# Kernel tuning notes

Measured on AMD Instinct MI355X. Metric: run time of the kernel, lower is better.

Reference implementation:

```python
import jax, jax.numpy as jnp
import numpy as np

B, L, H, C = 1, 512, 1024, 2


def setup_inputs() -> dict:
    key = jax.random.key(0)
    k1, k2, k3 = jax.random.split(key, 3)
    lm_output = jax.random.normal(k1, (B, L, H), dtype=jnp.float32)
    # torch Linear weight layout: [out_features, in_features]
    W1 = jax.random.normal(k2, (H, 2 * H), dtype=jnp.float32) * 0.02
    b1 = jnp.zeros((H,), dtype=jnp.float32)
    W2 = jax.random.normal(k3, (C, H), dtype=jnp.float32) * 0.02
    b2 = jnp.zeros((C,), dtype=jnp.float32)
    return {"lm_output": lm_output, "W1": W1, "b1": b1, "W2": W2, "b2": b2}


def reference(lm_output, W1, b1, W2, b2):
    # pair_emb[b,i,j] = concat(lm_output[b,j], lm_output[b,i])
    # Linear(concat(a,b)) decomposes: split W1 into the halves acting on each part.
    Wa = W1[:, :H]  # acts on lm_output_a (the j / column token)
    Wb = W1[:, H:]  # acts on lm_output_b (the i / row token)
    a_proj = jnp.einsum('blh,oh->blo', lm_output, Wa)  # [B,L,H]
    b_proj = jnp.einsum('blh,oh->blo', lm_output, Wb)  # [B,L,H]
    # hidden[b,i,j] = tanh(a_proj[b,j] + b_proj[b,i] + b1)   -> [B,L,L,H]
    hidden = jnp.tanh(a_proj[:, None, :, :] + b_proj[:, :, None, :] + b1)
    # Dropout is identity at inference time.
    logits = jnp.einsum('bijh,ch->bijc', hidden, W2) + b2  # [B,L,L,C]
    logits = (logits + jnp.swapaxes(logits, 1, 2)) / 2.0
    return logits
```

## Files before the change

kernel.cpp:

```cpp
#include <hip/hip_runtime.h>
#include <hip/hip_bf16.h>

#define HH 1024
#define LL 512
#define NT 16
#define NTRI 136

typedef __attribute__((ext_vector_type(8))) short bf16x8;
typedef __attribute__((ext_vector_type(4))) float f32x4;
typedef __attribute__((ext_vector_type(2))) float f32x2;

static constexpr float C_EXP = 2.8853900817779268f;

static __device__ __forceinline__ uint4 pack8(float4 a, float4 b) {
    union { uint4 u; __hip_bfloat162 h[4]; } r;
    r.h[0] = __float22bfloat162_rn(make_float2(a.x, a.y));
    r.h[1] = __float22bfloat162_rn(make_float2(a.z, a.w));
    r.h[2] = __float22bfloat162_rn(make_float2(b.x, b.y));
    r.h[3] = __float22bfloat162_rn(make_float2(b.z, b.w));
    return r.u;
}

__global__ __launch_bounds__(256, 4) void proj_mfma_kernel(
    const float* __restrict__ lm, const float* __restrict__ W1,
    const float* __restrict__ b1, float* __restrict__ Ea, float* __restrict__ Eb)
{
    __shared__ ushort As[64][136];
    __shared__ ushort Bs[64][136];

    const int tid  = threadIdx.x;
    const int lane = tid & 63;
    const int w    = tid >> 6;
    const int b    = blockIdx.x;
    const int xcd  = b & 7;
    const int idx  = b >> 3;
    const int nbase = (xcd * 4 + (idx & 3)) * 64;
    const int mbase = (idx >> 2) * 64;
    const int wm   = w * 16;
    const int sel  = nbase >> 10;
    const int nrow = nbase & 1023;

    const int frow = lane & 15;
    const int q8   = (lane >> 4) * 8;

    f32x4 acc[4] = {};

    for (int kb = 0; kb < HH; kb += 128) {
        __syncthreads();
        {
            int p = tid;
#pragma unroll
            for (int it = 0; it < 4; ++it, p += 256) {
                const int row = p >> 4, c8 = (p & 15) * 8;
                const float* pa = &lm[(mbase + row) * HH + kb + c8];
                *(uint4*)&As[row][c8] = pack8(*(const float4*)pa, *(const float4*)(pa + 4));
                const float* pw = &W1[(nrow + row) * 2048 + sel * 1024 + kb + c8];
                *(uint4*)&Bs[row][c8] = pack8(*(const float4*)pw, *(const float4*)(pw + 4));
            }
        }
        __syncthreads();

#pragma unroll
        for (int s = 0; s < 4; ++s) {
            const bf16x8 a = *(const bf16x8*)&As[wm + frow][s * 32 + q8];
#pragma unroll
            for (int nf = 0; nf < 4; ++nf) {
                const bf16x8 bb = *(const bf16x8*)&Bs[nf * 16 + frow][s * 32 + q8];
                acc[nf] = __builtin_amdgcn_mfma_f32_16x16x32_bf16(a, bb, acc[nf], 0, 0, 0);
            }
        }
    }

    const int col = lane & 15;
    const int rq  = (lane >> 4) * 4;
    const int m0  = mbase + wm + rq;
    const bool isA = sel == 0;
#pragma unroll
    for (int nf = 0; nf < 4; ++nf) {
        const int nn = (nrow + nf * 16 + col);
        if (isA) {
            const float bb = b1[nn];
#pragma unroll
            for (int r = 0; r < 4; ++r)
                Ea[(m0 + r) * HH + nn] = __builtin_amdgcn_exp2f(C_EXP * (acc[nf][r] + bb));
        } else {
#pragma unroll
            for (int r = 0; r < 4; ++r)
                Eb[(m0 + r) * HH + nn] = __builtin_amdgcn_exp2f(C_EXP * acc[nf][r]);
        }
    }
}

__global__ __launch_bounds__(256, 4) void pair_kernel(
    const float* __restrict__ Ea, const float* __restrict__ Eb,
    const float* __restrict__ W2, float* __restrict__ pbuf, int slice)
{
    __shared__ float eaj[32][68];
    __shared__ float eai[32][68];
    __shared__ float ebi[32][68];
    __shared__ float ebj[32][68];
    __shared__ f32x2 ws2[128];

    const int tid = threadIdx.x;
    const int tx  = tid & 15;
    const int ty  = tid >> 4;

    int tt = blockIdx.x, bi = 0, rem = NT;
    while (tt >= rem) { tt -= rem; --rem; ++bi; }
    const int bj    = bi + tt;
    const int ibase = bi * 32;
    const int jbase = bj * 32;
    const int k0    = blockIdx.y * slice;

    if (tid < slice)
        ws2[tid] = (f32x2){W2[k0 + tid], W2[HH + k0 + tid]};

    f32x2 acc2[2][2] = {};
    const f32x2 one2 = {1.f, 1.f};

    for (int kb = 0; kb < slice; kb += 64) {
        __syncthreads();
        {
            int p = tid;
#pragma unroll
            for (int it = 0; it < 8; ++it, p += 256) {
                const int tile = p >> 9;
                const int row  = (p >> 4) & 31;
                const int c4   = p & 15;
                float4 v;
                if      (tile == 0) v = *(const float4*)&Ea[(jbase + row) * HH + k0 + kb + c4 * 4];
                else if (tile == 1) v = *(const float4*)&Ea[(ibase + row) * HH + k0 + kb + c4 * 4];
                else if (tile == 2) v = *(const float4*)&Eb[(ibase + row) * HH + k0 + kb + c4 * 4];
                else                v = *(const float4*)&Eb[(jbase + row) * HH + k0 + kb + c4 * 4];
                if      (tile == 0) *(float4*)&eaj[row][c4 * 4] = v;
                else if (tile == 1) *(float4*)&eai[row][c4 * 4] = v;
                else if (tile == 2) *(float4*)&ebi[row][c4 * 4] = v;
                else                *(float4*)&ebj[row][c4 * 4] = v;
            }
        }
        __syncthreads();

#pragma unroll 4
        for (int h4 = 0; h4 < 16; ++h4) {
            const float4 Aj0 = *(const float4*)&eaj[tx][h4 * 4];
            const float4 Aj1 = *(const float4*)&eaj[tx + 16][h4 * 4];
            const float4 Bi0 = *(const float4*)&ebi[ty][h4 * 4];
            const float4 Bi1 = *(const float4*)&ebi[ty + 16][h4 * 4];
            const float4 Ai0 = *(const float4*)&eai[ty][h4 * 4];
            const float4 Ai1 = *(const float4*)&eai[ty + 16][h4 * 4];
            const float4 Bj0 = *(const float4*)&ebj[tx][h4 * 4];
            const float4 Bj1 = *(const float4*)&ebj[tx + 16][h4 * 4];
            const f32x4 wA = *(const f32x4*)&ws2[kb + h4 * 4];
            const f32x4 wB = *(const f32x4*)&ws2[kb + h4 * 4 + 2];

#define DO_H(AJ0v, AJ1v, BI0v, BI1v, AI0v, AI1v, BJ0v, BJ1v, W01)            \
            {                                                                 \
                const f32x2 Aj = {AJ0v, AJ1v};                                \
                const f32x2 Bj = {BJ0v, BJ1v};                                \
                const f32x2 d0 = __builtin_elementwise_fma((f32x2){BI0v, BI0v}, Aj, one2); \
                const f32x2 d1 = __builtin_elementwise_fma((f32x2){BI1v, BI1v}, Aj, one2); \
                const f32x2 e0 = __builtin_elementwise_fma((f32x2){AI0v, AI0v}, Bj, one2); \
                const f32x2 e1 = __builtin_elementwise_fma((f32x2){AI1v, AI1v}, Bj, one2); \
                const float dp0 = d0.x * d0.y, dp1 = d1.x * d1.y;             \
                const float ep0 = e0.x * e0.y, ep1 = e1.x * e1.y;             \
                const float DR = __builtin_amdgcn_rcpf(dp0 * dp1);            \
                const float ER = __builtin_amdgcn_rcpf(ep0 * ep1);            \
                const f32x2 dq = (f32x2){DR, DR} * (f32x2){dp1, dp0};         \
                const f32x2 eq = (f32x2){ER, ER} * (f32x2){ep1, ep0};         \
                const f32x2 u0 = (f32x2){dq.x, dq.x} * d0.yx + (f32x2){eq.x, eq.x} * e0.yx; \
                const f32x2 u1 = (f32x2){dq.y, dq.y} * d1.yx + (f32x2){eq.y, eq.y} * e1.yx; \
                acc2[0][0] = __builtin_elementwise_fma((f32x2){u0.x, u0.x}, (W01), acc2[0][0]); \
                acc2[0][1] = __builtin_elementwise_fma((f32x2){u0.y, u0.y}, (W01), acc2[0][1]); \
                acc2[1][0] = __builtin_elementwise_fma((f32x2){u1.x, u1.x}, (W01), acc2[1][0]); \
                acc2[1][1] = __builtin_elementwise_fma((f32x2){u1.y, u1.y}, (W01), acc2[1][1]); \
            }
            DO_H(Aj0.x, Aj1.x, Bi0.x, Bi1.x, Ai0.x, Ai1.x, Bj0.x, Bj1.x, wA.xy)
            DO_H(Aj0.y, Aj1.y, Bi0.y, Bi1.y, Ai0.y, Ai1.y, Bj0.y, Bj1.y, wA.zw)
            DO_H(Aj0.z, Aj1.z, Bi0.z, Bi1.z, Ai0.z, Ai1.z, Bj0.z, Bj1.z, wB.xy)
            DO_H(Aj0.w, Aj1.w, Bi0.w, Bi1.w, Ai0.w, Ai1.w, Bj0.w, Bj1.w, wB.zw)
#undef DO_H
        }
    }

    float* pb = pbuf + ((size_t)blockIdx.y * NTRI + blockIdx.x) * 2048;
#pragma unroll
    for (int ii = 0; ii < 2; ++ii)
#pragma unroll
        for (int jj = 0; jj < 2; ++jj) {
            const int li = ty + ii * 16, lj = tx + jj * 16;
            *(f32x2*)&pb[(li * 32 + lj) * 2] = acc2[ii][jj];
        }
}

__global__ __launch_bounds__(256) void combine_kernel(
    const float* __restrict__ pbuf, const float* __restrict__ W2,
    const float* __restrict__ b2, float* __restrict__ out, int nz)
{
    __shared__ float s_ws[2];

    const int tid = threadIdx.x;
    if (tid < 128) {
        const int c = tid >> 6, l = tid & 63;
        float s = 0.f;
#pragma unroll
        for (int q = 0; q < 4; ++q) {
            const float4 v = *(const float4*)&W2[c * HH + (l + q * 64) * 4];
            s += v.x + v.y + v.z + v.w;
        }
#pragma unroll
        for (int off = 32; off; off >>= 1) s += __shfl_down(s, off, 64);
        if (l == 0) s_ws[c] = s + b2[c];
    }
    __syncthreads();

    const int idx   = blockIdx.x * 256 + tid;
    const int t     = idx >> 11;
    const int local = idx & 2047;
    int tt = t, bi = 0, rem = NT;
    while (tt >= rem) { tt -= rem; --rem; ++bi; }
    const int bj = bi + tt;

    float s0 = 0.f, s1 = 0.f;
    for (int z = 0; z < nz; z += 2) {
        s0 += pbuf[((size_t)z * NTRI + t) * 2048 + local];
        s1 += pbuf[((size_t)(z + 1) * NTRI + t) * 2048 + local];
    }
    const float s = s0 + s1;

    const int li = local >> 6;
    const int lj = (local >> 1) & 31;
    const int c  = local & 1;
    const float v = s_ws[c] - s;

    const int i = bi * 32 + li;
    const int j = bj * 32 + lj;
    out[(i * LL + j) * 2 + c] = v;
    out[(j * LL + i) * 2 + c] = v;
}

extern "C" void kernel_launch(void* const* d_in, const int* in_sizes, int n_in,
                              void* d_out, int out_size, void* d_ws, size_t ws_size,
                              hipStream_t stream)
{
    const float* lm = (const float*)d_in[0];
    const float* W1 = (const float*)d_in[1];
    const float* b1 = (const float*)d_in[2];
    const float* W2 = (const float*)d_in[3];
    const float* b2 = (const float*)d_in[4];
    float* out = (float*)d_out;

    char* ws = (char*)d_ws;
    float* Ea   = (float*)ws;
    float* Eb   = (float*)(ws + (2u << 20));
    float* pbuf = (float*)(ws + (4u << 20) + 64);

    const size_t ubase = (4u << 20) + 64;
    const size_t pb16  = (size_t)16 * NTRI * 2048 * 4;
    const int nz = (ws_size >= ubase + pb16) ? 16 : 8;
    const int slice = HH / nz;

    proj_mfma_kernel<<<256, 256, 0, stream>>>(lm, W1, b1, Ea, Eb);
    pair_kernel<<<dim3(NTRI, nz), 256, 0, stream>>>(Ea, Eb, W2, pbuf, slice);
    combine_kernel<<<(NTRI * 2048) / 256, 256, 0, stream>>>(pbuf, W2, b2, out, nz);
}
```

Baseline: 129.4 us.

## Swizzle pair-kernel LDS tiles, read W2 from global, raise occupancy

Replaces the four padded 32x68 LDS tiles with one unpadded 4x32x64 array and XOR-swizzles the j-indexed tiles to avoid bank conflicts without padding. It drops the W2 staging in shared memory and loads W2 values straight from global memory inside the inner loop. It reorganizes the accumulators so packed FMAs pair along the output index rather than the class index, skips the first barrier, and raises the occupancy hint from 4 to 5 blocks per SIMD. This trades LDS footprint and bank conflicts for extra global (likely cached) W2 loads and tighter register pressure.

```diff
diff --git a/kernel.cpp b/kernel.cpp
--- a/kernel.cpp
+++ b/kernel.cpp
@@ -91,15 +91,11 @@
     }
 }
 
-__global__ __launch_bounds__(256, 4) void pair_kernel(
+__global__ __launch_bounds__(256, 5) void pair_kernel(
     const float* __restrict__ Ea, const float* __restrict__ Eb,
     const float* __restrict__ W2, float* __restrict__ pbuf, int slice)
 {
-    __shared__ float eaj[32][68];
-    __shared__ float eai[32][68];
-    __shared__ float ebi[32][68];
-    __shared__ float ebj[32][68];
-    __shared__ f32x2 ws2[128];
+    __shared__ float tl[4][32][64];
 
     const int tid = threadIdx.x;
     const int tx  = tid & 15;
@@ -112,14 +108,11 @@
     const int jbase = bj * 32;
     const int k0    = blockIdx.y * slice;
 
-    if (tid < slice)
-        ws2[tid] = (f32x2){W2[k0 + tid], W2[HH + k0 + tid]};
-
-    f32x2 acc2[2][2] = {};
+    f32x2 aC0[2] = {}, aC1[2] = {};
     const f32x2 one2 = {1.f, 1.f};
 
     for (int kb = 0; kb < slice; kb += 64) {
-        __syncthreads();
+        if (kb) __syncthreads();
         {
             int p = tid;
 #pragma unroll
@@ -132,52 +125,51 @@
                 else if (tile == 1) v = *(const float4*)&Ea[(ibase + row) * HH + k0 + kb + c4 * 4];
                 else if (tile == 2) v = *(const float4*)&Eb[(ibase + row) * HH + k0 + kb + c4 * 4];
                 else                v = *(const float4*)&Eb[(jbase + row) * HH + k0 + kb + c4 * 4];
-                if      (tile == 0) *(float4*)&eaj[row][c4 * 4] = v;
-                else if (tile == 1) *(float4*)&eai[row][c4 * 4] = v;
-                else if (tile == 2) *(float4*)&ebi[row][c4 * 4] = v;
-                else                *(float4*)&ebj[row][c4 * 4] = v;
+                const int c4s = (tile == 0 || tile == 3) ? (c4 ^ (row & 15)) : c4;
+                *(float4*)&tl[tile][row][c4s * 4] = v;
             }
         }
         __syncthreads();
 
 #pragma unroll 4
         for (int h4 = 0; h4 < 16; ++h4) {
-            const float4 Aj0 = *(const float4*)&eaj[tx][h4 * 4];
-            const float4 Aj1 = *(const float4*)&eaj[tx + 16][h4 * 4];
-            const float4 Bi0 = *(const float4*)&ebi[ty][h4 * 4];
-            const float4 Bi1 = *(const float4*)&ebi[ty + 16][h4 * 4];
-            const float4 Ai0 = *(const float4*)&eai[ty][h4 * 4];
-            const float4 Ai1 = *(const float4*)&eai[ty + 16][h4 * 4];
-            const float4 Bj0 = *(const float4*)&ebj[tx][h4 * 4];
-            const float4 Bj1 = *(const float4*)&ebj[tx + 16][h4 * 4];
-            const f32x4 wA = *(const f32x4*)&ws2[kb + h4 * 4];
-            const f32x4 wB = *(const f32x4*)&ws2[kb + h4 * 4 + 2];
-
-#define DO_H(AJ0v, AJ1v, BI0v, BI1v, AI0v, AI1v, BJ0v, BJ1v, W01)            \
-            {                                                                 \
-                const f32x2 Aj = {AJ0v, AJ1v};                                \
-                const f32x2 Bj = {BJ0v, BJ1v};                                \
+            const int sx = (h4 ^ tx) * 4;
+            const float4 Aj0 = *(const float4*)&tl[0][tx][sx];
+            const float4 Aj1 = *(const float4*)&tl[0][tx + 16][sx];
+            const float4 Bj0 = *(const float4*)&tl[3][tx][sx];
+            const float4 Bj1 = *(const float4*)&tl[3][tx + 16][sx];
+            const float4 Ai0 = *(const float4*)&tl[1][ty][h4 * 4];
+            const float4 Ai1 = *(const float4*)&tl[1][ty + 16][h4 * 4];
+            const float4 Bi0 = *(const float4*)&tl[2][ty][h4 * 4];
+            const float4 Bi1 = *(const float4*)&tl[2][ty + 16][h4 * 4];
+            const float4 w0q = *(const float4*)&W2[k0 + kb + h4 * 4];
+            const float4 w1q = *(const float4*)&W2[HH + k0 + kb + h4 * 4];
+
+#define DO_H(AJ0v, AJ1v, BI0v, BI1v, AI0v, AI1v, BJ0v, BJ1v, W0s, W1s)        \
+            {                                                                  \
+                const f32x2 Aj = {AJ0v, AJ1v};                                 \
+                const f32x2 Bj = {BJ0v, BJ1v};                                 \
                 const f32x2 d0 = __builtin_elementwise_fma((f32x2){BI0v, BI0v}, Aj, one2); \
                 const f32x2 d1 = __builtin_elementwise_fma((f32x2){BI1v, BI1v}, Aj, one2); \
                 const f32x2 e0 = __builtin_elementwise_fma((f32x2){AI0v, AI0v}, Bj, one2); \
                 const f32x2 e1 = __builtin_elementwise_fma((f32x2){AI1v, AI1v}, Bj, one2); \
-                const float dp0 = d0.x * d0.y, dp1 = d1.x * d1.y;             \
-                const float ep0 = e0.x * e0.y, ep1 = e1.x * e1.y;             \
-                const float DR = __builtin_amdgcn_rcpf(dp0 * dp1);            \
-                const float ER = __builtin_amdgcn_rcpf(ep0 * ep1);            \
-                const f32x2 dq = (f32x2){DR, DR} * (f32x2){dp1, dp0};         \
-                const f32x2 eq = (f32x2){ER, ER} * (f32x2){ep1, ep0};         \
+                const float dp0 = d0.x * d0.y, dp1 = d1.x * d1.y;              \
+                const float ep0 = e0.x * e0.y, ep1 = e1.x * e1.y;              \
+                const float DR = __builtin_amdgcn_rcpf(dp0 * dp1);             \
+                const float ER = __builtin_amdgcn_rcpf(ep0 * ep1);             \
+                const f32x2 dq = (f32x2){DR, DR} * (f32x2){dp1, dp0};          \
+                const f32x2 eq = (f32x2){ER, ER} * (f32x2){ep1, ep0};          \
                 const f32x2 u0 = (f32x2){dq.x, dq.x} * d0.yx + (f32x2){eq.x, eq.x} * e0.yx; \
                 const f32x2 u1 = (f32x2){dq.y, dq.y} * d1.yx + (f32x2){eq.y, eq.y} * e1.yx; \
-                acc2[0][0] = __builtin_elementwise_fma((f32x2){u0.x, u0.x}, (W01), acc2[0][0]); \
-                acc2[0][1] = __builtin_elementwise_fma((f32x2){u0.y, u0.y}, (W01), acc2[0][1]); \
-                acc2[1][0] = __builtin_elementwise_fma((f32x2){u1.x, u1.x}, (W01), acc2[1][0]); \
-                acc2[1][1] = __builtin_elementwise_fma((f32x2){u1.y, u1.y}, (W01), acc2[1][1]); \
-            }
-            DO_H(Aj0.x, Aj1.x, Bi0.x, Bi1.x, Ai0.x, Ai1.x, Bj0.x, Bj1.x, wA.xy)
-            DO_H(Aj0.y, Aj1.y, Bi0.y, Bi1.y, Ai0.y, Ai1.y, Bj0.y, Bj1.y, wA.zw)
-            DO_H(Aj0.z, Aj1.z, Bi0.z, Bi1.z, Ai0.z, Ai1.z, Bj0.z, Bj1.z, wB.xy)
-            DO_H(Aj0.w, Aj1.w, Bi0.w, Bi1.w, Ai0.w, Ai1.w, Bj0.w, Bj1.w, wB.zw)
+                aC0[0] = __builtin_elementwise_fma(u0, (f32x2){(W0s), (W0s)}, aC0[0]); \
+                aC1[0] = __builtin_elementwise_fma(u0, (f32x2){(W1s), (W1s)}, aC1[0]); \
+                aC0[1] = __builtin_elementwise_fma(u1, (f32x2){(W0s), (W0s)}, aC0[1]); \
+                aC1[1] = __builtin_elementwise_fma(u1, (f32x2){(W1s), (W1s)}, aC1[1]); \
+            }
+            DO_H(Aj0.x, Aj1.x, Bi0.x, Bi1.x, Ai0.x, Ai1.x, Bj0.x, Bj1.x, w0q.x, w1q.x)
+            DO_H(Aj0.y, Aj1.y, Bi0.y, Bi1.y, Ai0.y, Ai1.y, Bj0.y, Bj1.y, w0q.y, w1q.y)
+            DO_H(Aj0.z, Aj1.z, Bi0.z, Bi1.z, Ai0.z, Ai1.z, Bj0.z, Bj1.z, w0q.z, w1q.z)
+            DO_H(Aj0.w, Aj1.w, Bi0.w, Bi1.w, Ai0.w, Ai1.w, Bj0.w, Bj1.w, w0q.w, w1q.w)
 #undef DO_H
         }
     }
@@ -188,7 +180,9 @@
 #pragma unroll
         for (int jj = 0; jj < 2; ++jj) {
             const int li = ty + ii * 16, lj = tx + jj * 16;
-            *(f32x2*)&pb[(li * 32 + lj) * 2] = acc2[ii][jj];
+            const f32x2 v = { jj ? aC0[ii].y : aC0[ii].x,
+                              jj ? aC1[ii].y : aC1[ii].x };
+            *(f32x2*)&pb[(li * 32 + lj) * 2] = v;
         }
 }
 
```

Result: no change. 129.2 us (-0.2%).
